# Kernel tuning notes

Measured on AMD Instinct MI355X. Metric: run time of the kernel, lower is better.

## Reference

```python
import jax, jax.numpy as jnp
import numpy as np

# Vanilla tanh-RNN (num_layers=1, batch_first) followed by tanh + dropout(eval: identity) + linear.

def setup_inputs() -> dict:
    key = jax.random.key(0)
    ks = jax.random.split(key, 7)
    B, T, I, H, C = 16384, 64, 64, 100, 40
    s_ih = 1.0 / np.sqrt(H)
    return {
        "x": jax.random.normal(ks[0], (B, T * I), dtype=jnp.float32),
        "W_ih": jax.random.normal(ks[1], (H, I), dtype=jnp.float32) * s_ih,
        "W_hh": jax.random.normal(ks[2], (H, H), dtype=jnp.float32) * s_ih,
        "b_ih": jax.random.normal(ks[3], (H,), dtype=jnp.float32) * s_ih,
        "b_hh": jax.random.normal(ks[4], (H,), dtype=jnp.float32) * s_ih,
        "fc_W": jax.random.normal(ks[5], (C, H), dtype=jnp.float32) * 0.1,
        "fc_b": jax.random.normal(ks[6], (C,), dtype=jnp.float32) * 0.1,
    }


def reference(x, W_ih, W_hh, b_ih, b_hh, fc_W, fc_b):
    B = x.shape[0]
    x = x.reshape(B, 64, 64)  # [B, T, I]
    # Precompute input projections for all steps in one GEMM: [B, T, H]
    xp = jnp.einsum("bti,hi->bth", x, W_ih) + b_ih + b_hh
    h0 = jnp.zeros((B, W_hh.shape[0]), dtype=x.dtype)

    def step(h, xp_t):  # h: [B, H], xp_t: [B, H]
        h_new = jnp.tanh(xp_t + h @ W_hh.T)
        return h_new, None

    h_last, _ = jax.lax.scan(step, h0, jnp.swapaxes(xp, 0, 1))  # scan over T
    out = jnp.tanh(h_last)  # tanh on last-step output
    # dropout(p=0.2) in eval mode = identity
    return out @ fc_W.T + fc_b  # [B, 40]
```

## Files before the change

kernel.cpp:

```cpp
#include <hip/hip_runtime.h>


typedef _Float16 half8 __attribute__((ext_vector_type(8)));
typedef float float4_t __attribute__((ext_vector_type(4)));
typedef unsigned int uint4_t __attribute__((ext_vector_type(4)));

#define ROW_BYTES 1088
#define BUF_BYTES (16 * ROW_BYTES)
#define GLOAD16(gp, lp)                                                   \
  __builtin_amdgcn_global_load_lds(                                       \
      (const __attribute__((address_space(1))) void*)(gp),                \
      (__attribute__((address_space(3))) void*)(lp), 16, 0, 0)

__device__ __forceinline__ float tanh_fast(float x) {
  float e = __builtin_amdgcn_exp2f(x * 2.8853900817779268f);
  return 1.0f - 2.0f * __builtin_amdgcn_rcpf(e + 1.0f);
}
__device__ __forceinline__ unsigned int pk2(float lo, float hi) {
  return __builtin_bit_cast(unsigned int, __builtin_amdgcn_cvt_pkrtz(lo, hi));
}
__device__ __forceinline__ half8 pack4(unsigned int a, unsigned int b,
                                       unsigned int c, unsigned int d) {
  uint4_t u = {a, b, c, d};
  return __builtin_bit_cast(half8, u);
}

__device__ __forceinline__ void issue_slab(const float* srcl, int slab, char* buf) {
  const float* s = srcl + slab * 256;
  #pragma unroll
  for (int j = 0; j < 16; ++j) {
    GLOAD16(s, buf + j * ROW_BYTES);
    s += 4096;
  }
}

__global__ __launch_bounds__(64, 1) void rnn_fused(
    const float* __restrict__ x, const float* __restrict__ W_ih,
    const float* __restrict__ W_hh, const float* __restrict__ b_ih,
    const float* __restrict__ b_hh, const float* __restrict__ fc_W,
    const float* __restrict__ fc_b, float* __restrict__ out, int B)
{
  __shared__ char xring[2 * BUF_BYTES];
  const int lane = threadIdx.x & 63;
  const int g = lane >> 4;
  const int c = lane & 15;
  const int rowbase = blockIdx.x * 16;

  const float* srcl = x + (size_t)rowbase * 4096 + lane * 4;
  issue_slab(srcl, 0, xring);
  issue_slab(srcl, 1, xring + BUF_BYTES);

  half8 wih[2][7];
  half8 whh[4][7];
  float4_t bias[7];

  #pragma unroll
  for (int nt = 0; nt < 7; ++nt) {
    int nb = nt * 16 + 4 * g;
    float4_t bi = {0.f, 0.f, 0.f, 0.f};
    if (nb + 3 < 100) {
      float4_t a = *(const float4_t*)(b_ih + nb);
      float4_t b = *(const float4_t*)(b_hh + nb);
      bi = a + b;
    }
    bias[nt] = bi;

    int nrow = nt * 16 + c;
    bool rv = (nrow < 100);
    #pragma unroll
    for (int kb = 0; kb < 2; ++kb) {
      float4_t f0 = {0.f,0.f,0.f,0.f}, f1 = {0.f,0.f,0.f,0.f};
      if (rv) {
        const float* p = W_ih + nrow * 64 + kb * 32 + g * 8;
        f0 = *(const float4_t*)p;
        f1 = *(const float4_t*)(p + 4);
      }
      half8 h;
      #pragma unroll
      for (int j = 0; j < 4; ++j) { h[2*j] = (_Float16)f0[j]; h[2*j+1] = (_Float16)f1[j]; }
      wih[kb][nt] = h;
    }
    #pragma unroll
    for (int kb = 0; kb < 4; ++kb) {
      int clo = kb * 32 + 4 * g;
      int chi = clo + 16;
      float4_t f0 = {0.f,0.f,0.f,0.f}, f1 = {0.f,0.f,0.f,0.f};
      if (rv && clo + 3 < 100) f0 = *(const float4_t*)(W_hh + nrow * 100 + clo);
      if (rv && chi + 3 < 100) f1 = *(const float4_t*)(W_hh + nrow * 100 + chi);
      half8 h;
      #pragma unroll
      for (int j = 0; j < 4; ++j) { h[2*j] = (_Float16)f0[j]; h[2*j+1] = (_Float16)f1[j]; }
      whh[kb][nt] = h;
    }
  }

  const unsigned ring_base =
      (unsigned)(uintptr_t)(__attribute__((address_space(3))) char*)xring;
  const unsigned xa0 = ring_base + (unsigned)(c * ROW_BYTES + g * 32);
  const float4_t fzero = {0.f, 0.f, 0.f, 0.f};

  float4_t accA[7], accB[7], accX[7];
  half8 hfrag[4];
  #pragma unroll
  for (int kb = 0; kb < 4; ++kb) hfrag[kb] = (half8)(_Float16)0.0f;

  for (int grp = 0; grp < 16; ++grp) {
    asm volatile("s_waitcnt vmcnt(16)" ::: "memory");
    unsigned xg = xa0 + (unsigned)((grp & 1) * BUF_BYTES);

    #pragma unroll
    for (int t4 = 0; t4 < 4; ++t4) {
      unsigned xs = xg + (unsigned)(t4 * 256);
      float4_t s0, s1, s2, s3;
      asm volatile(
          "ds_read_b128 %0, %4 offset:0\n\t"
          "ds_read_b128 %1, %4 offset:16\n\t"
          "ds_read_b128 %2, %4 offset:128\n\t"
          "ds_read_b128 %3, %4 offset:144"
          : "=&v"(s0), "=&v"(s1), "=&v"(s2), "=&v"(s3)
          : "v"(xs) : "memory");

      #pragma unroll
      for (int nt = 0; nt < 7; ++nt)
        accA[nt] = __builtin_amdgcn_mfma_f32_16x16x32_f16(whh[0][nt], hfrag[0], bias[nt], 0, 0, 0);
      #pragma unroll
      for (int nt = 0; nt < 7; ++nt)
        accB[nt] = __builtin_amdgcn_mfma_f32_16x16x32_f16(whh[2][nt], hfrag[2], fzero, 0, 0, 0);

      asm volatile("s_waitcnt lgkmcnt(0)"
                   : "+v"(s0), "+v"(s1), "+v"(s2), "+v"(s3) :: "memory");
      __builtin_amdgcn_sched_barrier(0);

      half8 xb0 = pack4(pk2(s0[0], s1[0]), pk2(s0[1], s1[1]),
                        pk2(s0[2], s1[2]), pk2(s0[3], s1[3]));
      half8 xb1 = pack4(pk2(s2[0], s3[0]), pk2(s2[1], s3[1]),
                        pk2(s2[2], s3[2]), pk2(s2[3], s3[3]));

      #pragma unroll
      for (int nt = 0; nt < 7; ++nt)
        accX[nt] = __builtin_amdgcn_mfma_f32_16x16x32_f16(wih[0][nt], xb0, fzero, 0, 0, 0);
      #pragma unroll
      for (int nt = 0; nt < 7; ++nt)
        accA[nt] = __builtin_amdgcn_mfma_f32_16x16x32_f16(whh[1][nt], hfrag[1], accA[nt], 0, 0, 0);
      #pragma unroll
      for (int nt = 0; nt < 7; ++nt)
        accB[nt] = __builtin_amdgcn_mfma_f32_16x16x32_f16(whh[3][nt], hfrag[3], accB[nt], 0, 0, 0);
      #pragma unroll
      for (int nt = 0; nt < 7; ++nt)
        accX[nt] = __builtin_amdgcn_mfma_f32_16x16x32_f16(wih[1][nt], xb1, accX[nt], 0, 0, 0);

      #pragma unroll
      for (int nt = 0; nt < 7; ++nt) {
        accA[nt] = (accA[nt] + accB[nt]) + accX[nt];
        #pragma unroll
        for (int v = 0; v < 4; ++v)
          accA[nt][v] = tanh_fast(accA[nt][v]);
      }

      #pragma unroll
      for (int kb = 0; kb < 3; ++kb)
        hfrag[kb] = pack4(pk2(accA[2*kb][0], accA[2*kb+1][0]),
                          pk2(accA[2*kb][1], accA[2*kb+1][1]),
                          pk2(accA[2*kb][2], accA[2*kb+1][2]),
                          pk2(accA[2*kb][3], accA[2*kb+1][3]));
      hfrag[3] = pack4(pk2(accA[6][0], 0.0f), pk2(accA[6][1], 0.0f),
                       pk2(accA[6][2], 0.0f), pk2(accA[6][3], 0.0f));
    }

    int sl = grp + 2; if (sl > 15) sl = 15;
    issue_slab(srcl, sl, xring + (grp & 1) * BUF_BYTES);
  }

  #pragma unroll
  for (int nt = 0; nt < 7; ++nt)
    #pragma unroll
    for (int v = 0; v < 4; ++v)
      accA[nt][v] = tanh_fast(accA[nt][v]);

  half8 zf[4];
  #pragma unroll
  for (int kb = 0; kb < 3; ++kb)
    zf[kb] = pack4(pk2(accA[2*kb][0], accA[2*kb+1][0]),
                   pk2(accA[2*kb][1], accA[2*kb+1][1]),
                   pk2(accA[2*kb][2], accA[2*kb+1][2]),
                   pk2(accA[2*kb][3], accA[2*kb+1][3]));
  zf[3] = pack4(pk2(accA[6][0], 0.0f), pk2(accA[6][1], 0.0f),
                pk2(accA[6][2], 0.0f), pk2(accA[6][3], 0.0f));

  half8 wfc[4][3];
  float4_t bfc[3];
  #pragma unroll
  for (int nt = 0; nt < 3; ++nt) {
    int nb = nt * 16 + 4 * g;
    float4_t bi = {0.f,0.f,0.f,0.f};
    if (nb + 3 < 40) bi = *(const float4_t*)(fc_b + nb);
    bfc[nt] = bi;

    int nrow = nt * 16 + c;
    bool rv = (nrow < 40);
    #pragma unroll
    for (int kb = 0; kb < 4; ++kb) {
      int clo = kb * 32 + 4 * g;
      int chi = clo + 16;
      float4_t f0 = {0.f,0.f,0.f,0.f}, f1 = {0.f,0.f,0.f,0.f};
      if (rv && clo + 3 < 100) f0 = *(const float4_t*)(fc_W + nrow * 100 + clo);
      if (rv && chi + 3 < 100) f1 = *(const float4_t*)(fc_W + nrow * 100 + chi);
      half8 h;
      #pragma unroll
      for (int j = 0; j < 4; ++j) {
        h[2 * j]     = (_Float16)f0[j];
        h[2 * j + 1] = (_Float16)f1[j];
      }
      wfc[kb][nt] = h;
    }
  }

  float4_t oacc[3];
  #pragma unroll
  for (int nt = 0; nt < 3; ++nt) oacc[nt] = bfc[nt];
  #pragma unroll
  for (int kb = 0; kb < 4; ++kb)
    #pragma unroll
    for (int nt = 0; nt < 3; ++nt)
      oacc[nt] = __builtin_amdgcn_mfma_f32_16x16x32_f16(wfc[kb][nt], zf[kb], oacc[nt], 0, 0, 0);

  #pragma unroll
  for (int nt = 0; nt < 3; ++nt)
    #pragma unroll
    for (int v = 0; v < 4; ++v) {
      int n = nt * 16 + 4 * g + v;
      if (n < 40)
        out[(size_t)(rowbase + c) * 40 + n] = oacc[nt][v];
    }
}

extern "C" void kernel_launch(void* const* d_in, const int* in_sizes, int n_in,
                              void* d_out, int out_size, void* d_ws, size_t ws_size,
                              hipStream_t stream) {
  const float* x    = (const float*)d_in[0];
  const float* W_ih = (const float*)d_in[1];
  const float* W_hh = (const float*)d_in[2];
  const float* b_ih = (const float*)d_in[3];
  const float* b_hh = (const float*)d_in[4];
  const float* fc_W = (const float*)d_in[5];
  const float* fc_b = (const float*)d_in[6];
  float* outp = (float*)d_out;

  int B = in_sizes[0] / 4096;
  int grid = (B + 15) / 16;
  rnn_fused<<<grid, 64, 0, stream>>>(x, W_ih, W_hh, b_ih, b_hh, fc_W, fc_b, outp, B);
}
```

Measured before the change: 79.18 us.

## Process two independent 16-row batch tiles per wave to hide recurrence latency

Each wave now handles 32 batch rows as two interleaved independent recurrences (A and B), so one tile's MFMA chain and tanh can overlap the other's dependency stalls. The earlier split of the hidden-state matmul into partial accumulators is replaced by a single serial chain per tile. The LDS staging drops row padding in favour of an XOR swizzle to avoid bank conflicts. The grid is halved, and LDS use and register pressure per wave roughly double, which may reduce occupancy and limit how many CUs are kept busy.

```diff
diff --git a/kernel.cpp b/kernel.cpp
--- a/kernel.cpp
+++ b/kernel.cpp
@@ -5,8 +5,8 @@
 typedef float float4_t __attribute__((ext_vector_type(4)));
 typedef unsigned int uint4_t __attribute__((ext_vector_type(4)));
 
-#define ROW_BYTES 1088
-#define BUF_BYTES (16 * ROW_BYTES)
+#define SLAB_BYTES 16384
+#define TILE_LDS   (2 * SLAB_BYTES)
 #define GLOAD16(gp, lp)                                                   \
   __builtin_amdgcn_global_load_lds(                                       \
       (const __attribute__((address_space(1))) void*)(gp),                \
@@ -25,12 +25,12 @@
   return __builtin_bit_cast(half8, u);
 }
 
-__device__ __forceinline__ void issue_slab(const float* srcl, int slab, char* buf) {
-  const float* s = srcl + slab * 256;
+__device__ __forceinline__ void issue_slab(const float* srcT, int slab,
+                                           char* buf, int lane) {
   #pragma unroll
   for (int j = 0; j < 16; ++j) {
-    GLOAD16(s, buf + j * ROW_BYTES);
-    s += 4096;
+    int loff = (lane * 4) ^ ((j & 3) << 3);
+    GLOAD16(srcT + (size_t)j * 4096 + slab * 256 + loff, buf + j * 1024);
   }
 }
 
@@ -40,20 +40,25 @@
     const float* __restrict__ b_hh, const float* __restrict__ fc_W,
     const float* __restrict__ fc_b, float* __restrict__ out, int B)
 {
-  __shared__ char xring[2 * BUF_BYTES];
+  __shared__ char xlds[2 * TILE_LDS];
   const int lane = threadIdx.x & 63;
   const int g = lane >> 4;
   const int c = lane & 15;
-  const int rowbase = blockIdx.x * 16;
-
-  const float* srcl = x + (size_t)rowbase * 4096 + lane * 4;
-  issue_slab(srcl, 0, xring);
-  issue_slab(srcl, 1, xring + BUF_BYTES);
+  const int rowbase = blockIdx.x * 32;
+
+  const float* srcA = x + (size_t)rowbase * 4096;
+  const float* srcB = srcA + (size_t)16 * 4096;
+  char* ldsA = xlds;
+  char* ldsB = xlds + TILE_LDS;
+
+  issue_slab(srcA, 0, ldsA, lane);
+  issue_slab(srcB, 0, ldsB, lane);
+  issue_slab(srcA, 1, ldsA + SLAB_BYTES, lane);
+  issue_slab(srcB, 1, ldsB + SLAB_BYTES, lane);
 
   half8 wih[2][7];
   half8 whh[4][7];
   float4_t bias[7];
-
   #pragma unroll
   for (int nt = 0; nt < 7; ++nt) {
     int nb = nt * 16 + 4 * g;
@@ -94,98 +99,144 @@
     }
   }
 
-  const unsigned ring_base =
-      (unsigned)(uintptr_t)(__attribute__((address_space(3))) char*)xring;
-  const unsigned xa0 = ring_base + (unsigned)(c * ROW_BYTES + g * 32);
-  const float4_t fzero = {0.f, 0.f, 0.f, 0.f};
-
-  float4_t accA[7], accB[7], accX[7];
-  half8 hfrag[4];
-  #pragma unroll
-  for (int kb = 0; kb < 4; ++kb) hfrag[kb] = (half8)(_Float16)0.0f;
+  const unsigned lb =
+      (unsigned)(uintptr_t)(__attribute__((address_space(3))) char*)xlds;
+  const unsigned baseA = lb + (unsigned)(c * 1024 + ((g * 32) ^ ((c & 3) << 5)));
+  const unsigned baseB = baseA + TILE_LDS;
+
+  float4_t accA[7], accB[7];
+  half8 hfA[4], hfB[4];
+  #pragma unroll
+  for (int kb = 0; kb < 4; ++kb) {
+    hfA[kb] = (half8)(_Float16)0.0f;
+    hfB[kb] = (half8)(_Float16)0.0f;
+  }
 
   for (int grp = 0; grp < 16; ++grp) {
-    asm volatile("s_waitcnt vmcnt(16)" ::: "memory");
-    unsigned xg = xa0 + (unsigned)((grp & 1) * BUF_BYTES);
+    asm volatile("s_waitcnt vmcnt(32)" ::: "memory");
+    const unsigned offg = (unsigned)((grp & 1) * SLAB_BYTES);
 
     #pragma unroll
     for (int t4 = 0; t4 < 4; ++t4) {
-      unsigned xs = xg + (unsigned)(t4 * 256);
-      float4_t s0, s1, s2, s3;
+      unsigned aA = baseA + offg + (unsigned)(t4 * 256);
+      unsigned aB = baseB + offg + (unsigned)(t4 * 256);
+      float4_t sa0, sa1, sa2, sa3, sb0, sb1, sb2, sb3;
       asm volatile(
           "ds_read_b128 %0, %4 offset:0\n\t"
           "ds_read_b128 %1, %4 offset:16\n\t"
           "ds_read_b128 %2, %4 offset:128\n\t"
           "ds_read_b128 %3, %4 offset:144"
-          : "=&v"(s0), "=&v"(s1), "=&v"(s2), "=&v"(s3)
-          : "v"(xs) : "memory");
+          : "=&v"(sa0), "=&v"(sa1), "=&v"(sa2), "=&v"(sa3)
+          : "v"(aA) : "memory");
+      asm volatile(
+          "ds_read_b128 %0, %4 offset:0\n\t"
+          "ds_read_b128 %1, %4 offset:16\n\t"
+          "ds_read_b128 %2, %4 offset:128\n\t"
+          "ds_read_b128 %3, %4 offset:144"
+          : "=&v"(sb0), "=&v"(sb1), "=&v"(sb2), "=&v"(sb3)
+          : "v"(aB) : "memory");
 
       #pragma unroll
       for (int nt = 0; nt < 7; ++nt)
-        accA[nt] = __builtin_amdgcn_mfma_f32_16x16x32_f16(whh[0][nt], hfrag[0], bias[nt], 0, 0, 0);
+        accA[nt] = __builtin_amdgcn_mfma_f32_16x16x32_f16(whh[0][nt], hfA[0], bias[nt], 0, 0, 0);
+      #pragma unroll
+      for (int kb = 1; kb < 4; ++kb)
+        #pragma unroll
+        for (int nt = 0; nt < 7; ++nt)
+          accA[nt] = __builtin_amdgcn_mfma_f32_16x16x32_f16(whh[kb][nt], hfA[kb], accA[nt], 0, 0, 0);
+
+      asm volatile("s_waitcnt lgkmcnt(4)"
+                   : "+v"(sa0), "+v"(sa1), "+v"(sa2), "+v"(sa3) :: "memory");
+      __builtin_amdgcn_sched_barrier(0);
+      half8 xa0 = pack4(pk2(sa0[0], sa1[0]), pk2(sa0[1], sa1[1]),
+                        pk2(sa0[2], sa1[2]), pk2(sa0[3], sa1[3]));
+      half8 xa1 = pack4(pk2(sa2[0], sa3[0]), pk2(sa2[1], sa3[1]),
+                        pk2(sa2[2], sa3[2]), pk2(sa2[3], sa3[3]));
+      #pragma unroll
+      for (int nt = 0; nt < 7; ++nt) {
+        accA[nt] = __builtin_amdgcn_mfma_f32_16x16x32_f16(wih[0][nt], xa0, accA[nt], 0, 0, 0);
+        accA[nt] = __builtin_amdgcn_mfma_f32_16x16x32_f16(wih[1][nt], xa1, accA[nt], 0, 0, 0);
+      }
+
       #pragma unroll
       for (int nt = 0; nt < 7; ++nt)
-        accB[nt] = __builtin_amdgcn_mfma_f32_16x16x32_f16(whh[2][nt], hfrag[2], fzero, 0, 0, 0);
+        accB[nt] = __builtin_amdgcn_mfma_f32_16x16x32_f16(whh[0][nt], hfB[0], bias[nt], 0, 0, 0);
+      #pragma unroll
+      for (int kb = 1; kb < 4; ++kb)
+        #pragma unroll
+        for (int nt = 0; nt < 7; ++nt)
+          accB[nt] = __builtin_amdgcn_mfma_f32_16x16x32_f16(whh[kb][nt], hfB[kb], accB[nt], 0, 0, 0);
 
       asm volatile("s_waitcnt lgkmcnt(0)"
-                   : "+v"(s0), "+v"(s1), "+v"(s2), "+v"(s3) :: "memory");
+                   : "+v"(sb0), "+v"(sb1), "+v"(sb2), "+v"(sb3) :: "memory");
       __builtin_amdgcn_sched_barrier(0);
-
-      half8 xb0 = pack4(pk2(s0[0], s1[0]), pk2(s0[1], s1[1]),
-                        pk2(s0[2], s1[2]), pk2(s0[3], s1[3]));
-      half8 xb1 = pack4(pk2(s2[0], s3[0]), pk2(s2[1], s3[1]),
-                        pk2(s2[2], s3[2]), pk2(s2[3], s3[3]));
+      half8 xb0 = pack4(pk2(sb0[0], sb1[0]), pk2(sb0[1], sb1[1]),
+                        pk2(sb0[2], sb1[2]), pk2(sb0[3], sb1[3]));
+      half8 xb1 = pack4(pk2(sb2[0], sb3[0]), pk2(sb2[1], sb3[1]),
+                        pk2(sb2[2], sb3[2]), pk2(sb2[3], sb3[3]));
+      #pragma unroll
+      for (int nt = 0; nt < 7; ++nt) {
+        accB[nt] = __builtin_amdgcn_mfma_f32_16x16x32_f16(wih[0][nt], xb0, accB[nt], 0, 0, 0);
+        accB[nt] = __builtin_amdgcn_mfma_f32_16x16x32_f16(wih[1][nt], xb1, accB[nt], 0, 0, 0);
+      }
 
       #pragma unroll
       for (int nt = 0; nt < 7; ++nt)
-        accX[nt] = __builtin_amdgcn_mfma_f32_16x16x32_f16(wih[0][nt], xb0, fzero, 0, 0, 0);
-      #pragma unroll
-      for (int nt = 0; nt < 7; ++nt)
-        accA[nt] = __builtin_amdgcn_mfma_f32_16x16x32_f16(whh[1][nt], hfrag[1], accA[nt], 0, 0, 0);
-      #pragma unroll
-      for (int nt = 0; nt < 7; ++nt)
-        accB[nt] = __builtin_amdgcn_mfma_f32_16x16x32_f16(whh[3][nt], hfrag[3], accB[nt], 0, 0, 0);
-      #pragma unroll
-      for (int nt = 0; nt < 7; ++nt)
-        accX[nt] = __builtin_amdgcn_mfma_f32_16x16x32_f16(wih[1][nt], xb1, accX[nt], 0, 0, 0);
-
-      #pragma unroll
-      for (int nt = 0; nt < 7; ++nt) {
-        accA[nt] = (accA[nt] + accB[nt]) + accX[nt];
         #pragma unroll
         for (int v = 0; v < 4; ++v)
           accA[nt][v] = tanh_fast(accA[nt][v]);
-      }
-
       #pragma unroll
       for (int kb = 0; kb < 3; ++kb)
-        hfrag[kb] = pack4(pk2(accA[2*kb][0], accA[2*kb+1][0]),
-                          pk2(accA[2*kb][1], accA[2*kb+1][1]),
-                          pk2(accA[2*kb][2], accA[2*kb+1][2]),
-                          pk2(accA[2*kb][3], accA[2*kb+1][3]));
-      hfrag[3] = pack4(pk2(accA[6][0], 0.0f), pk2(accA[6][1], 0.0f),
-                       pk2(accA[6][2], 0.0f), pk2(accA[6][3], 0.0f));
+        hfA[kb] = pack4(pk2(accA[2*kb][0], accA[2*kb+1][0]),
+                        pk2(accA[2*kb][1], accA[2*kb+1][1]),
+                        pk2(accA[2*kb][2], accA[2*kb+1][2]),
+                        pk2(accA[2*kb][3], accA[2*kb+1][3]));
+      hfA[3] = pack4(pk2(accA[6][0], 0.0f), pk2(accA[6][1], 0.0f),
+                     pk2(accA[6][2], 0.0f), pk2(accA[6][3], 0.0f));
+
+      #pragma unroll
+      for (int nt = 0; nt < 7; ++nt)
+        #pragma unroll
+        for (int v = 0; v < 4; ++v)
+          accB[nt][v] = tanh_fast(accB[nt][v]);
+      #pragma unroll
+      for (int kb = 0; kb < 3; ++kb)
+        hfB[kb] = pack4(pk2(accB[2*kb][0], accB[2*kb+1][0]),
+                        pk2(accB[2*kb][1], accB[2*kb+1][1]),
+                        pk2(accB[2*kb][2], accB[2*kb+1][2]),
+                        pk2(accB[2*kb][3], accB[2*kb+1][3]));
+      hfB[3] = pack4(pk2(accB[6][0], 0.0f), pk2(accB[6][1], 0.0f),
+                     pk2(accB[6][2], 0.0f), pk2(accB[6][3], 0.0f));
     }
 
     int sl = grp + 2; if (sl > 15) sl = 15;
-    issue_slab(srcl, sl, xring + (grp & 1) * BUF_BYTES);
-  }
-
+    issue_slab(srcA, sl, ldsA + (sl & 1) * SLAB_BYTES, lane);
+    issue_slab(srcB, sl, ldsB + (sl & 1) * SLAB_BYTES, lane);
+  }
+
+  half8 zfA[4], zfB[4];
   #pragma unroll
   for (int nt = 0; nt < 7; ++nt)
     #pragma unroll
-    for (int v = 0; v < 4; ++v)
+    for (int v = 0; v < 4; ++v) {
       accA[nt][v] = tanh_fast(accA[nt][v]);
-
-  half8 zf[4];
-  #pragma unroll
-  for (int kb = 0; kb < 3; ++kb)
-    zf[kb] = pack4(pk2(accA[2*kb][0], accA[2*kb+1][0]),
-                   pk2(accA[2*kb][1], accA[2*kb+1][1]),
-                   pk2(accA[2*kb][2], accA[2*kb+1][2]),
-                   pk2(accA[2*kb][3], accA[2*kb+1][3]));
-  zf[3] = pack4(pk2(accA[6][0], 0.0f), pk2(accA[6][1], 0.0f),
-                pk2(accA[6][2], 0.0f), pk2(accA[6][3], 0.0f));
+      accB[nt][v] = tanh_fast(accB[nt][v]);
+    }
+  #pragma unroll
+  for (int kb = 0; kb < 3; ++kb) {
+    zfA[kb] = pack4(pk2(accA[2*kb][0], accA[2*kb+1][0]),
+                    pk2(accA[2*kb][1], accA[2*kb+1][1]),
+                    pk2(accA[2*kb][2], accA[2*kb+1][2]),
+                    pk2(accA[2*kb][3], accA[2*kb+1][3]));
+    zfB[kb] = pack4(pk2(accB[2*kb][0], accB[2*kb+1][0]),
+                    pk2(accB[2*kb][1], accB[2*kb+1][1]),
+                    pk2(accB[2*kb][2], accB[2*kb+1][2]),
+                    pk2(accB[2*kb][3], accB[2*kb+1][3]));
+  }
+  zfA[3] = pack4(pk2(accA[6][0], 0.0f), pk2(accA[6][1], 0.0f),
+                 pk2(accA[6][2], 0.0f), pk2(accA[6][3], 0.0f));
+  zfB[3] = pack4(pk2(accB[6][0], 0.0f), pk2(accB[6][1], 0.0f),
+                 pk2(accB[6][2], 0.0f), pk2(accB[6][3], 0.0f));
 
   half8 wfc[4][3];
   float4_t bfc[3];
@@ -207,30 +258,31 @@
       if (rv && chi + 3 < 100) f1 = *(const float4_t*)(fc_W + nrow * 100 + chi);
       half8 h;
       #pragma unroll
-      for (int j = 0; j < 4; ++j) {
-        h[2 * j]     = (_Float16)f0[j];
-        h[2 * j + 1] = (_Float16)f1[j];
-      }
+      for (int j = 0; j < 4; ++j) { h[2*j] = (_Float16)f0[j]; h[2*j+1] = (_Float16)f1[j]; }
       wfc[kb][nt] = h;
     }
   }
 
-  float4_t oacc[3];
-  #pragma unroll
-  for (int nt = 0; nt < 3; ++nt) oacc[nt] = bfc[nt];
+  float4_t oaccA[3], oaccB[3];
+  #pragma unroll
+  for (int nt = 0; nt < 3; ++nt) { oaccA[nt] = bfc[nt]; oaccB[nt] = bfc[nt]; }
   #pragma unroll
   for (int kb = 0; kb < 4; ++kb)
     #pragma unroll
-    for (int nt = 0; nt < 3; ++nt)
-      oacc[nt] = __builtin_amdgcn_mfma_f32_16x16x32_f16(wfc[kb][nt], zf[kb], oacc[nt], 0, 0, 0);
+    for (int nt = 0; nt < 3; ++nt) {
+      oaccA[nt] = __builtin_amdgcn_mfma_f32_16x16x32_f16(wfc[kb][nt], zfA[kb], oaccA[nt], 0, 0, 0);
+      oaccB[nt] = __builtin_amdgcn_mfma_f32_16x16x32_f16(wfc[kb][nt], zfB[kb], oaccB[nt], 0, 0, 0);
+    }
 
   #pragma unroll
   for (int nt = 0; nt < 3; ++nt)
     #pragma unroll
     for (int v = 0; v < 4; ++v) {
       int n = nt * 16 + 4 * g + v;
-      if (n < 40)
-        out[(size_t)(rowbase + c) * 40 + n] = oacc[nt][v];
+      if (n < 40) {
+        out[(size_t)(rowbase + c) * 40 + n] = oaccA[nt][v];
+        out[(size_t)(rowbase + 16 + c) * 40 + n] = oaccB[nt][v];
+      }
     }
 }
 
@@ -247,6 +299,6 @@
   float* outp = (float*)d_out;
 
   int B = in_sizes[0] / 4096;
-  int grid = (B + 15) / 16;
+  int grid = (B + 31) / 32;
   rnn_fused<<<grid, 64, 0, stream>>>(x, W_ih, W_hh, b_ih, b_hh, fc_W, fc_b, outp, B);
 }
```

Result: slower. 118.5 us (+49.7%).
